# Optimization experiments

Hardware: AMD Instinct MI355X
Metric: run time of the kernel (lower is better)

The kernel has to match this reference:

```python
import jax, jax.numpy as jnp
import numpy as np

EMBED = 1024
HEADS = 16
HEAD_DIM = EMBED // HEADS


def setup_inputs() -> dict:
    key = jax.random.key(0)
    ks = jax.random.split(key, 8)
    N, L = 4, 2048
    values = jax.random.normal(ks[0], (N, L, EMBED), dtype=jnp.float32)
    keys_ = jax.random.normal(ks[1], (N, L, EMBED), dtype=jnp.float32)
    queries = jax.random.normal(ks[2], (N, L, EMBED), dtype=jnp.float32)
    s = 1.0 / np.sqrt(HEAD_DIM)
    Wv = jax.random.normal(ks[3], (HEAD_DIM, HEAD_DIM), dtype=jnp.float32) * s
    Wk = jax.random.normal(ks[4], (HEAD_DIM, HEAD_DIM), dtype=jnp.float32) * s
    Wq = jax.random.normal(ks[5], (HEAD_DIM, HEAD_DIM), dtype=jnp.float32) * s
    Wo = jax.random.normal(ks[6], (EMBED, EMBED), dtype=jnp.float32) * (1.0 / np.sqrt(EMBED))
    bo = jnp.zeros((EMBED,), dtype=jnp.float32)
    return {"values": values, "keys": keys_, "queries": queries,
            "Wv": Wv, "Wk": Wk, "Wq": Wq, "Wo": Wo, "bo": bo}


def reference(values, keys, queries, Wv, Wk, Wq, Wo, bo):
    N, L, _ = queries.shape
    # split heads: [N, L, H, D]
    v = values.reshape(N, -1, HEADS, HEAD_DIM)
    k = keys.reshape(N, -1, HEADS, HEAD_DIM)
    q = queries.reshape(N, L, HEADS, HEAD_DIM)
    # per-head linear (same [D,D] weight shared across heads), torch Linear: x @ W.T
    v = jnp.einsum('nlhd,ed->nlhe', v, Wv)
    k = jnp.einsum('nlhd,ed->nlhe', k, Wk)
    q = jnp.einsum('nqhd,ed->nqhe', q, Wq)
    # attention scores [N, H, Q, K], scaled by sqrt(embed_size) as in source
    scores = jnp.einsum('nqhd,nkhd->nhqk', q, k) / jnp.sqrt(jnp.float32(EMBED))
    attn = jax.nn.softmax(scores, axis=-1)
    out = jnp.einsum('nhqk,nkhd->nqhd', attn, v).reshape(N, L, EMBED)
    return out @ Wo.T + bo
```

## Files before the change

### kernel.cpp

```cpp
#include <hip/hip_runtime.h>
#include <math.h>

#define EMBED 1024
#define HEADS 16
#define HD    64
#define NB    4
#define LSEQ  2048

typedef __attribute__((ext_vector_type(8))) short bf16x8;
typedef __attribute__((ext_vector_type(16))) float f32x16;

typedef __attribute__((address_space(1))) void as1_void;
typedef __attribute__((address_space(3))) void as3_void;

__device__ __forceinline__ void gload_lds16(const void* g, void* l) {
    __builtin_amdgcn_global_load_lds((const as1_void*)g, (as3_void*)l, 16, 0, 0);
}

__device__ inline bf16x8 as_bf16x8(uint4 u) {
    union { uint4 u; bf16x8 b; } c; c.u = u; return c.b;
}
__device__ inline unsigned short bf16r(float x) {
    unsigned u = __float_as_uint(x);
    u += 0x7fffu + ((u >> 16) & 1u);
    return (unsigned short)(u >> 16);
}
__device__ inline float bfh2f(unsigned short h) {
    return __uint_as_float(((unsigned)h) << 16);
}
__device__ inline void split2(float x, float y, unsigned& hw, unsigned& lw) {
    unsigned short hx = bf16r(x), hy = bf16r(y);
    unsigned short lx = bf16r(x - bfh2f(hx)), ly = bf16r(y - bfh2f(hy));
    hw = (unsigned)hx | ((unsigned)hy << 16);
    lw = (unsigned)lx | ((unsigned)ly << 16);
}

__global__ __launch_bounds__(256, 3) void proj_kernel(
    const float* __restrict__ Xv, const float* __restrict__ Xk, const float* __restrict__ Xq,
    const float* __restrict__ Wv, const float* __restrict__ Wk, const float* __restrict__ Wq,
    unsigned short* __restrict__ Vt, unsigned short* __restrict__ Kp, unsigned short* __restrict__ Qp)
{
    __shared__ uint4 sXh[128 * 8];
    __shared__ uint4 sXl[128 * 8];
    __shared__ uint4 sWh[64 * 8];
    __shared__ uint4 sWl[64 * 8];

    const int t = threadIdx.x;
    const int lane = t & 63, w = t >> 6;
    const int l5 = lane & 31, hi = lane >> 5;
    const int h  = blockIdx.y;
    const int n  = blockIdx.x >> 4;
    const int l0 = (blockIdx.x & 15) * 128;

    const float QSC = 1.44269504088896341f / 32.0f;
    const float* Xs[3] = {Xv, Xk, Xq};
    const float* Ws[3] = {Wv, Wk, Wq};

    const int frow = t >> 4;
    const int fcol = t & 15;

    for (int p = 0; p < 3; ++p) {
        __syncthreads();
        {
            const float* xb = Xs[p] + ((size_t)(n * LSEQ + l0 + frow)) * EMBED + h * HD + fcol * 4;
            unsigned short* dh = (unsigned short*)sXh;
            unsigned short* dl = (unsigned short*)sXl;
            #pragma unroll
            for (int i = 0; i < 8; ++i) {
                int row = frow + i * 16;
                float4 v = *(const float4*)(xb + (size_t)i * 16 * EMBED);
                int gg = fcol >> 1, s8 = (fcol & 1) * 4;
                int idx = row * 64 + ((gg ^ (row & 7)) * 8) + s8;
                uint2 hv, lv;
                split2(v.x, v.y, hv.x, lv.x);
                split2(v.z, v.w, hv.y, lv.y);
                *(uint2*)(dh + idx) = hv;
                *(uint2*)(dl + idx) = lv;
            }
        }
        #pragma unroll
        for (int i = 0; i < 2; ++i) {
            int u = t + 256 * i;
            int e = u >> 3, g = u & 7;
            const float* wb = Ws[p] + u * 8;
            float4 v0 = *(const float4*)(wb);
            float4 v1 = *(const float4*)(wb + 4);
            uint4 hq, lq;
            split2(v0.x, v0.y, hq.x, lq.x);
            split2(v0.z, v0.w, hq.y, lq.y);
            split2(v1.x, v1.y, hq.z, lq.z);
            split2(v1.z, v1.w, hq.w, lq.w);
            int idx = e * 8 + (g ^ (e & 7));
            sWh[idx] = hq;
            sWl[idx] = lq;
        }
        __syncthreads();

        f32x16 acc0, acc1;
        #pragma unroll
        for (int i = 0; i < 16; ++i) { acc0[i] = 0.f; acc1[i] = 0.f; }

        const int xrow = w * 32 + l5;
        const int w0r = l5, w1r = 32 + l5;
        #pragma unroll
        for (int kc = 0; kc < 4; ++kc) {
            int gsel = kc * 2 + hi;
            bf16x8 xh = as_bf16x8(sXh[xrow * 8 + (gsel ^ (xrow & 7))]);
            bf16x8 xl = as_bf16x8(sXl[xrow * 8 + (gsel ^ (xrow & 7))]);
            bf16x8 wh0 = as_bf16x8(sWh[w0r * 8 + (gsel ^ (w0r & 7))]);
            bf16x8 wl0 = as_bf16x8(sWl[w0r * 8 + (gsel ^ (w0r & 7))]);
            bf16x8 wh1 = as_bf16x8(sWh[w1r * 8 + (gsel ^ (w1r & 7))]);
            bf16x8 wl1 = as_bf16x8(sWl[w1r * 8 + (gsel ^ (w1r & 7))]);
            if (p == 0) {
                acc0 = __builtin_amdgcn_mfma_f32_32x32x16_bf16(wh0, xh, acc0, 0, 0, 0);
                acc0 = __builtin_amdgcn_mfma_f32_32x32x16_bf16(wh0, xl, acc0, 0, 0, 0);
                acc0 = __builtin_amdgcn_mfma_f32_32x32x16_bf16(wl0, xh, acc0, 0, 0, 0);
                acc1 = __builtin_amdgcn_mfma_f32_32x32x16_bf16(wh1, xh, acc1, 0, 0, 0);
                acc1 = __builtin_amdgcn_mfma_f32_32x32x16_bf16(wh1, xl, acc1, 0, 0, 0);
                acc1 = __builtin_amdgcn_mfma_f32_32x32x16_bf16(wl1, xh, acc1, 0, 0, 0);
            } else {
                acc0 = __builtin_amdgcn_mfma_f32_32x32x16_bf16(xh, wh0, acc0, 0, 0, 0);
                acc0 = __builtin_amdgcn_mfma_f32_32x32x16_bf16(xh, wl0, acc0, 0, 0, 0);
                acc0 = __builtin_amdgcn_mfma_f32_32x32x16_bf16(xl, wh0, acc0, 0, 0, 0);
                acc1 = __builtin_amdgcn_mfma_f32_32x32x16_bf16(xh, wh1, acc1, 0, 0, 0);
                acc1 = __builtin_amdgcn_mfma_f32_32x32x16_bf16(xh, wl1, acc1, 0, 0, 0);
                acc1 = __builtin_amdgcn_mfma_f32_32x32x16_bf16(xl, wh1, acc1, 0, 0, 0);
            }
        }

        if (p == 0) {
            unsigned short* vb = Vt + (((size_t)(n * HEADS + h)) * HD) * LSEQ + l0 + w * 32 + l5;
            #pragma unroll
            for (int r = 0; r < 16; ++r) {
                int er = (r & 3) + 8 * (r >> 2) + 4 * hi;
                vb[(size_t)er * LSEQ]        = bf16r(acc0[r]);
                vb[(size_t)(32 + er) * LSEQ] = bf16r(acc1[r]);
            }
        } else {
            unsigned short* dst = (p == 1) ? Kp : Qp;
            float sc = (p == 2) ? QSC : 1.0f;
            unsigned short* db = dst + (((size_t)(n * HEADS + h)) * LSEQ + l0 + w * 32) * HD;
            #pragma unroll
            for (int r = 0; r < 16; ++r) {
                int tok = (r & 3) + 8 * (r >> 2) + 4 * hi;
                db[(size_t)tok * HD + l5]      = bf16r(acc0[r] * sc);
                db[(size_t)tok * HD + 32 + l5] = bf16r(acc1[r] * sc);
            }
        }
    }
}

__global__ __launch_bounds__(256, 4) void attn_kernel(
    const unsigned short* __restrict__ Qp, const unsigned short* __restrict__ Kp,
    const unsigned short* __restrict__ Vt,
    unsigned short* __restrict__ AOh, unsigned short* __restrict__ AOl)
{
    __shared__ uint4 sK[2][64 * 8];
    __shared__ uint4 sV[2][64 * 8];

    const int t = threadIdx.x;
    const int lane = t & 63, w = t >> 6;
    const int l5 = lane & 31, hi = lane >> 5;
    const int n = blockIdx.z, h = blockIdx.y;
    const int q0 = blockIdx.x * 128;
    const size_t hoff = ((size_t)n * HEADS + h) * (size_t)(LSEQ * HD);
    const unsigned short* Kh = Kp + hoff;
    const unsigned short* Vh = Vt + hoff;

    bf16x8 qf[4];
    {
        const uint4* qg = (const uint4*)(Qp + hoff + (size_t)(q0 + w * 32 + l5) * HD);
        #pragma unroll
        for (int kc = 0; kc < 4; ++kc) qf[kc] = as_bf16x8(qg[kc * 2 + hi]);
    }

    f32x16 Oa0, Oa1;
    #pragma unroll
    for (int i = 0; i < 16; ++i) { Oa0[i] = 0.f; Oa1[i] = 0.f; }
    float ls0 = 0.f, ls1 = 0.f;

    const int r0 = t >> 3;
    const int g0 = (t & 7) ^ (r0 & 7);
    const uint4* gK = (const uint4*)Kh;
    const uint4* gV = (const uint4*)Vh;

    #define STAGE(TILE, BUF)                                                        \
        do {                                                                        \
            int kb_ = (TILE) * 64;                                                  \
            gload_lds16(gK + (size_t)(kb_ + r0) * 8 + g0,        &sK[BUF][t]);      \
            gload_lds16(gK + (size_t)(kb_ + r0 + 32) * 8 + g0,   &sK[BUF][t + 256]);\
            gload_lds16(gV + (size_t)r0 * 256 + (kb_ >> 3) + g0, &sV[BUF][t]);      \
            gload_lds16(gV + (size_t)(r0 + 32) * 256 + (kb_ >> 3) + g0,             \
                        &sV[BUF][t + 256]);                                         \
        } while (0)

    STAGE(0, 0);
    int cur = 0;

    for (int tt = 0; tt < LSEQ / 64; ++tt) {
        if (tt + 1 < LSEQ / 64) {
            STAGE(tt + 1, cur ^ 1);
            asm volatile("s_waitcnt vmcnt(4)" ::: "memory");
        } else {
            asm volatile("s_waitcnt vmcnt(0)" ::: "memory");
        }
        __builtin_amdgcn_s_barrier();

        #pragma unroll
        for (int tc = 0; tc < 2; ++tc) {
            f32x16 c;
            #pragma unroll
            for (int i = 0; i < 16; ++i) c[i] = 0.f;
            int key = tc * 32 + l5;
            __builtin_amdgcn_s_setprio(1);
            #pragma unroll
            for (int kc = 0; kc < 4; ++kc) {
                bf16x8 kf = as_bf16x8(sK[cur][key * 8 + ((kc * 2 + hi) ^ (l5 & 7))]);
                c = __builtin_amdgcn_mfma_f32_32x32x16_bf16(kf, qf[kc], c, 0, 0, 0);
            }
            __builtin_amdgcn_s_setprio(0);

            unsigned pw[8];
            #pragma unroll
            for (int g = 0; g < 4; ++g) {
                float p0 = exp2f(c[4 * g]);
                float p1 = exp2f(c[4 * g + 1]);
                float p2 = exp2f(c[4 * g + 2]);
                float p3 = exp2f(c[4 * g + 3]);
                ls0 += (p0 + p1);
                ls1 += (p2 + p3);
                asm("v_cvt_pk_bf16_f32 %0, %1, %2" : "=v"(pw[2 * g])     : "v"(p0), "v"(p1));
                asm("v_cvt_pk_bf16_f32 %0, %1, %2" : "=v"(pw[2 * g + 1]) : "v"(p2), "v"(p3));
            }
            asm("v_permlane32_swap_b32 %0, %1" : "+v"(pw[0]), "+v"(pw[2]));
            asm("v_permlane32_swap_b32 %0, %1" : "+v"(pw[1]), "+v"(pw[3]));
            asm("v_permlane32_swap_b32 %0, %1" : "+v"(pw[4]), "+v"(pw[6]));
            asm("v_permlane32_swap_b32 %0, %1" : "+v"(pw[5]), "+v"(pw[7]));

            __builtin_amdgcn_s_setprio(1);
            #pragma unroll
            for (int win = 0; win < 2; ++win) {
                union { unsigned u[4]; bf16x8 b; } pf;
                pf.u[0] = pw[4 * win];
                pf.u[1] = pw[4 * win + 1];
                pf.u[2] = pw[4 * win + 2];
                pf.u[3] = pw[4 * win + 3];
                int vg = tc * 4 + (win << 1) + hi;
                bf16x8 v0 = as_bf16x8(sV[cur][ l5       * 8 + (vg ^ (l5 & 7))]);
                Oa0 = __builtin_amdgcn_mfma_f32_32x32x16_bf16(pf.b, v0, Oa0, 0, 0, 0);
                bf16x8 v1 = as_bf16x8(sV[cur][(32 + l5) * 8 + (vg ^ (l5 & 7))]);
                Oa1 = __builtin_amdgcn_mfma_f32_32x32x16_bf16(pf.b, v1, Oa1, 0, 0, 0);
            }
            __builtin_amdgcn_s_setprio(0);
        }
        __builtin_amdgcn_s_barrier();
        cur ^= 1;
    }
    #undef STAGE

    float lsum = ls0 + ls1;
    lsum += __shfl_xor(lsum, 32);
    float inv = 1.0f / lsum;
    float* sLf = (float*)&sK[0][0];
    if (hi == 0) sLf[w * 32 + l5] = inv;
    __syncthreads();

    unsigned short* hB = AOh + hoff;
    unsigned short* lB = AOl + hoff;
    #pragma unroll
    for (int r = 0; r < 16; ++r) {
        int qr = (r & 3) + 8 * (r >> 2) + 4 * hi;
        float invq = sLf[w * 32 + qr];
        size_t row = (size_t)(q0 + w * 32 + qr) * HD;
        float o0 = Oa0[r] * invq;
        float o1 = Oa1[r] * invq;
        unsigned short h0 = bf16r(o0), h1 = bf16r(o1);
        hB[row +      l5] = h0;
        hB[row + 32 + l5] = h1;
        lB[row +      l5] = bf16r(o0 - bfh2f(h0));
        lB[row + 32 + l5] = bf16r(o1 - bfh2f(h1));
    }
}

__global__ __launch_bounds__(256) void wsplit_kernel(
    const float* __restrict__ Wo,
    unsigned short* __restrict__ Woh, unsigned short* __restrict__ Wol)
{
    int i = blockIdx.x * 256 + threadIdx.x;
    float4 v = ((const float4*)Wo)[i];
    ushort4 h, l;
    h.x = bf16r(v.x); l.x = bf16r(v.x - bfh2f(h.x));
    h.y = bf16r(v.y); l.y = bf16r(v.y - bfh2f(h.y));
    h.z = bf16r(v.z); l.z = bf16r(v.z - bfh2f(h.z));
    h.w = bf16r(v.w); l.w = bf16r(v.w - bfh2f(h.w));
    ((ushort4*)Woh)[i] = h;
    ((ushort4*)Wol)[i] = l;
}

__global__ __launch_bounds__(256, 2) void outproj_kernel(
    const unsigned short* __restrict__ AOh, const unsigned short* __restrict__ AOl,
    const unsigned short* __restrict__ Woh, const unsigned short* __restrict__ Wol,
    const float* __restrict__ bo, float* __restrict__ out)
{
    __shared__ uint4 sAh[1024];
    __shared__ uint4 sAl[1024];
    __shared__ uint4 sBh[1024];
    __shared__ uint4 sBl[1024];

    const int t = threadIdx.x;
    const int lane = t & 63, w = t >> 6;
    const int l5 = lane & 31, hi = lane >> 5;
    const int m0 = blockIdx.x * 128;
    const int e0 = blockIdx.y * 128;
    const int n  = m0 >> 11, l0 = m0 & 2047;
    const int mr = (w & 1) * 64, nc = (w >> 1) * 64;

    f32x16 acc[2][2];
    #pragma unroll
    for (int a = 0; a < 2; ++a)
        #pragma unroll
        for (int b = 0; b < 2; ++b)
            #pragma unroll
            for (int i = 0; i < 16; ++i) acc[a][b][i] = 0.f;

    for (int hh = 0; hh < 16; ++hh) {
        const unsigned short* Ah = AOh + ((((size_t)n * HEADS + hh) * LSEQ) + l0) * HD;
        const unsigned short* Al = AOl + ((((size_t)n * HEADS + hh) * LSEQ) + l0) * HD;
        #pragma unroll
        for (int i = 0; i < 4; ++i) {
            int g = t + i * 256;
            gload_lds16(Ah + g * 8, sAh + g);
            gload_lds16(Al + g * 8, sAl + g);
            int e = g >> 3, gf = g & 7;
            size_t boff = (size_t)(e0 + e) * EMBED + hh * 64 + gf * 8;
            gload_lds16(Woh + boff, sBh + g);
            gload_lds16(Wol + boff, sBl + g);
        }
        __syncthreads();

        #pragma unroll
        for (int s = 0; s < 4; ++s) {
            int gcol = s * 2 + hi;
            bf16x8 ah0 = as_bf16x8(sAh[(mr +      l5) * 8 + gcol]);
            bf16x8 ah1 = as_bf16x8(sAh[(mr + 32 + l5) * 8 + gcol]);
            bf16x8 al0 = as_bf16x8(sAl[(mr +      l5) * 8 + gcol]);
            bf16x8 al1 = as_bf16x8(sAl[(mr + 32 + l5) * 8 + gcol]);
            bf16x8 bh0 = as_bf16x8(sBh[(nc +      l5) * 8 + gcol]);
            bf16x8 bh1 = as_bf16x8(sBh[(nc + 32 + l5) * 8 + gcol]);
            bf16x8 bl0 = as_bf16x8(sBl[(nc +      l5) * 8 + gcol]);
            bf16x8 bl1 = as_bf16x8(sBl[(nc + 32 + l5) * 8 + gcol]);

            acc[0][0] = __builtin_amdgcn_mfma_f32_32x32x16_bf16(ah0, bh0, acc[0][0], 0, 0, 0);
            acc[0][1] = __builtin_amdgcn_mfma_f32_32x32x16_bf16(ah0, bh1, acc[0][1], 0, 0, 0);
            acc[1][0] = __builtin_amdgcn_mfma_f32_32x32x16_bf16(ah1, bh0, acc[1][0], 0, 0, 0);
            acc[1][1] = __builtin_amdgcn_mfma_f32_32x32x16_bf16(ah1, bh1, acc[1][1], 0, 0, 0);

            acc[0][0] = __builtin_amdgcn_mfma_f32_32x32x16_bf16(ah0, bl0, acc[0][0], 0, 0, 0);
            acc[0][1] = __builtin_amdgcn_mfma_f32_32x32x16_bf16(ah0, bl1, acc[0][1], 0, 0, 0);
            acc[1][0] = __builtin_amdgcn_mfma_f32_32x32x16_bf16(ah1, bl0, acc[1][0], 0, 0, 0);
            acc[1][1] = __builtin_amdgcn_mfma_f32_32x32x16_bf16(ah1, bl1, acc[1][1], 0, 0, 0);

            acc[0][0] = __builtin_amdgcn_mfma_f32_32x32x16_bf16(al0, bh0, acc[0][0], 0, 0, 0);
            acc[0][1] = __builtin_amdgcn_mfma_f32_32x32x16_bf16(al0, bh1, acc[0][1], 0, 0, 0);
            acc[1][0] = __builtin_amdgcn_mfma_f32_32x32x16_bf16(al1, bh0, acc[1][0], 0, 0, 0);
            acc[1][1] = __builtin_amdgcn_mfma_f32_32x32x16_bf16(al1, bh1, acc[1][1], 0, 0, 0);
        }
        __syncthreads();
    }

    float b0 = bo[e0 + nc + l5];
    float b1 = bo[e0 + nc + 32 + l5];
    #pragma unroll
    for (int ti = 0; ti < 2; ++ti) {
        #pragma unroll
        for (int r = 0; r < 16; ++r) {
            int row = m0 + mr + ti * 32 + (r & 3) + 8 * (r >> 2) + 4 * hi;
            float* o = out + (size_t)row * EMBED + e0 + nc;
            o[l5]      = acc[ti][0][r] + b0;
            o[32 + l5] = acc[ti][1][r] + b1;
        }
    }
}

extern "C" void kernel_launch(void* const* d_in, const int* in_sizes, int n_in,
                              void* d_out, int out_size, void* d_ws, size_t ws_size,
                              hipStream_t stream)
{
    const float* values  = (const float*)d_in[0];
    const float* keys    = (const float*)d_in[1];
    const float* queries = (const float*)d_in[2];
    const float* Wv      = (const float*)d_in[3];
    const float* Wk      = (const float*)d_in[4];
    const float* Wq      = (const float*)d_in[5];
    const float* Wo      = (const float*)d_in[6];
    const float* bo      = (const float*)d_in[7];
    float* out = (float*)d_out;

    const size_t bufElems = (size_t)NB * HEADS * LSEQ * HD;
    unsigned short* Qp  = (unsigned short*)d_ws;
    unsigned short* Kp  = Qp  + bufElems;
    unsigned short* Vt  = Kp  + bufElems;
    unsigned short* AOh = Vt  + bufElems;
    unsigned short* AOl = AOh + bufElems;
    unsigned short* Woh = AOl + bufElems;
    unsigned short* Wol = Woh + (size_t)EMBED * EMBED;

    wsplit_kernel<<<dim3(1024), 256, 0, stream>>>(Wo, Woh, Wol);
    proj_kernel<<<dim3(NB * 16, HEADS), 256, 0, stream>>>(values, keys, queries, Wv, Wk, Wq, Vt, Kp, Qp);
    attn_kernel<<<dim3(LSEQ / 128, HEADS, NB), 256, 0, stream>>>(Qp, Kp, Vt, AOh, AOl);
    outproj_kernel<<<dim3(NB * LSEQ / 128, EMBED / 128), 256, 0, stream>>>(AOh, AOl, Woh, Wol, bo, out);
}
```

Measured before the change: 377.9 us.

## Double-buffer out-projection LDS stages and prefetch next QKV projection inputs

The output-projection GEMM now splits each head's K=64 slice into two 32-wide chunks and double-buffers them in LDS. The next chunk's global-to-LDS loads are issued before computing the current one, with vmcnt-based waits and an XOR swizzle to reduce bank conflicts. The QKV projection kernel prefetches the next projection's X and W tiles into registers while the current one computes. This trades extra registers and a subtler barrier/waitcnt protocol for hiding global load latency.

```diff
diff --git a/kernel.cpp b/kernel.cpp
--- a/kernel.cpp
+++ b/kernel.cpp
@@ -59,21 +59,34 @@
     const int frow = t >> 4;
     const int fcol = t & 15;
 
+    float4 xr[8];
+    float4 wr[4];
+
+    {
+        const float* xb = Xs[0] + ((size_t)(n * LSEQ + l0 + frow)) * EMBED + h * HD + fcol * 4;
+        #pragma unroll
+        for (int i = 0; i < 8; ++i) xr[i] = *(const float4*)(xb + (size_t)i * 16 * EMBED);
+        const float* wb0 = Ws[0] + (size_t)t * 8;
+        const float* wb1 = Ws[0] + (size_t)(t + 256) * 8;
+        wr[0] = *(const float4*)(wb0);
+        wr[1] = *(const float4*)(wb0 + 4);
+        wr[2] = *(const float4*)(wb1);
+        wr[3] = *(const float4*)(wb1 + 4);
+    }
+
     for (int p = 0; p < 3; ++p) {
         __syncthreads();
         {
-            const float* xb = Xs[p] + ((size_t)(n * LSEQ + l0 + frow)) * EMBED + h * HD + fcol * 4;
             unsigned short* dh = (unsigned short*)sXh;
             unsigned short* dl = (unsigned short*)sXl;
             #pragma unroll
             for (int i = 0; i < 8; ++i) {
                 int row = frow + i * 16;
-                float4 v = *(const float4*)(xb + (size_t)i * 16 * EMBED);
                 int gg = fcol >> 1, s8 = (fcol & 1) * 4;
                 int idx = row * 64 + ((gg ^ (row & 7)) * 8) + s8;
                 uint2 hv, lv;
-                split2(v.x, v.y, hv.x, lv.x);
-                split2(v.z, v.w, hv.y, lv.y);
+                split2(xr[i].x, xr[i].y, hv.x, lv.x);
+                split2(xr[i].z, xr[i].w, hv.y, lv.y);
                 *(uint2*)(dh + idx) = hv;
                 *(uint2*)(dl + idx) = lv;
             }
@@ -82,19 +95,28 @@
         for (int i = 0; i < 2; ++i) {
             int u = t + 256 * i;
             int e = u >> 3, g = u & 7;
-            const float* wb = Ws[p] + u * 8;
-            float4 v0 = *(const float4*)(wb);
-            float4 v1 = *(const float4*)(wb + 4);
             uint4 hq, lq;
-            split2(v0.x, v0.y, hq.x, lq.x);
-            split2(v0.z, v0.w, hq.y, lq.y);
-            split2(v1.x, v1.y, hq.z, lq.z);
-            split2(v1.z, v1.w, hq.w, lq.w);
+            split2(wr[2 * i].x, wr[2 * i].y, hq.x, lq.x);
+            split2(wr[2 * i].z, wr[2 * i].w, hq.y, lq.y);
+            split2(wr[2 * i + 1].x, wr[2 * i + 1].y, hq.z, lq.z);
+            split2(wr[2 * i + 1].z, wr[2 * i + 1].w, hq.w, lq.w);
             int idx = e * 8 + (g ^ (e & 7));
             sWh[idx] = hq;
             sWl[idx] = lq;
         }
-        __syncthreads();
+        if (p < 2) {
+            const float* xb = Xs[p + 1] + ((size_t)(n * LSEQ + l0 + frow)) * EMBED + h * HD + fcol * 4;
+            #pragma unroll
+            for (int i = 0; i < 8; ++i) xr[i] = *(const float4*)(xb + (size_t)i * 16 * EMBED);
+            const float* wb0 = Ws[p + 1] + (size_t)t * 8;
+            const float* wb1 = Ws[p + 1] + (size_t)(t + 256) * 8;
+            wr[0] = *(const float4*)(wb0);
+            wr[1] = *(const float4*)(wb0 + 4);
+            wr[2] = *(const float4*)(wb1);
+            wr[3] = *(const float4*)(wb1 + 4);
+        }
+        asm volatile("s_waitcnt lgkmcnt(0)" ::: "memory");
+        __builtin_amdgcn_s_barrier();
 
         f32x16 acc0, acc1;
         #pragma unroll
@@ -302,10 +324,10 @@
     const unsigned short* __restrict__ Woh, const unsigned short* __restrict__ Wol,
     const float* __restrict__ bo, float* __restrict__ out)
 {
-    __shared__ uint4 sAh[1024];
-    __shared__ uint4 sAl[1024];
-    __shared__ uint4 sBh[1024];
-    __shared__ uint4 sBl[1024];
+    __shared__ uint4 sAh[2][512];
+    __shared__ uint4 sAl[2][512];
+    __shared__ uint4 sBh[2][512];
+    __shared__ uint4 sBl[2][512];
 
     const int t = threadIdx.x;
     const int lane = t & 63, w = t >> 6;
@@ -315,6 +337,28 @@
     const int n  = m0 >> 11, l0 = m0 & 2047;
     const int mr = (w & 1) * 64, nc = (w >> 1) * 64;
 
+    const int ar0 = t >> 2;
+    const int ag0 = (t & 3) ^ (ar0 & 3);
+
+    #define OSTAGE(C, BUF)                                                            \
+        do {                                                                          \
+            int hh_ = (C) >> 1, hf_ = (C) & 1;                                        \
+            const uint4* gAh_ = (const uint4*)(AOh) +                                 \
+                (((size_t)n * HEADS + hh_) * LSEQ + l0) * 8;                          \
+            const uint4* gAl_ = (const uint4*)(AOl) +                                 \
+                (((size_t)n * HEADS + hh_) * LSEQ + l0) * 8;                          \
+            const uint4* gBh_ = (const uint4*)(Woh) + (size_t)e0 * 128 + hh_ * 8;     \
+            const uint4* gBl_ = (const uint4*)(Wol) + (size_t)e0 * 128 + hh_ * 8;     \
+            gload_lds16(gAh_ + (size_t)ar0 * 8 + hf_ * 4 + ag0,        &sAh[BUF][t]);       \
+            gload_lds16(gAh_ + (size_t)(ar0 + 64) * 8 + hf_ * 4 + ag0, &sAh[BUF][t + 256]); \
+            gload_lds16(gAl_ + (size_t)ar0 * 8 + hf_ * 4 + ag0,        &sAl[BUF][t]);       \
+            gload_lds16(gAl_ + (size_t)(ar0 + 64) * 8 + hf_ * 4 + ag0, &sAl[BUF][t + 256]); \
+            gload_lds16(gBh_ + (size_t)ar0 * 128 + hf_ * 4 + ag0,        &sBh[BUF][t]);       \
+            gload_lds16(gBh_ + (size_t)(ar0 + 64) * 128 + hf_ * 4 + ag0, &sBh[BUF][t + 256]); \
+            gload_lds16(gBl_ + (size_t)ar0 * 128 + hf_ * 4 + ag0,        &sBl[BUF][t]);       \
+            gload_lds16(gBl_ + (size_t)(ar0 + 64) * 128 + hf_ * 4 + ag0, &sBl[BUF][t + 256]); \
+        } while (0)
+
     f32x16 acc[2][2];
     #pragma unroll
     for (int a = 0; a < 2; ++a)
@@ -323,32 +367,30 @@
             #pragma unroll
             for (int i = 0; i < 16; ++i) acc[a][b][i] = 0.f;
 
-    for (int hh = 0; hh < 16; ++hh) {
-        const unsigned short* Ah = AOh + ((((size_t)n * HEADS + hh) * LSEQ) + l0) * HD;
-        const unsigned short* Al = AOl + ((((size_t)n * HEADS + hh) * LSEQ) + l0) * HD;
-        #pragma unroll
-        for (int i = 0; i < 4; ++i) {
-            int g = t + i * 256;
-            gload_lds16(Ah + g * 8, sAh + g);
-            gload_lds16(Al + g * 8, sAl + g);
-            int e = g >> 3, gf = g & 7;
-            size_t boff = (size_t)(e0 + e) * EMBED + hh * 64 + gf * 8;
-            gload_lds16(Woh + boff, sBh + g);
-            gload_lds16(Wol + boff, sBl + g);
-        }
-        __syncthreads();
-
-        #pragma unroll
-        for (int s = 0; s < 4; ++s) {
-            int gcol = s * 2 + hi;
-            bf16x8 ah0 = as_bf16x8(sAh[(mr +      l5) * 8 + gcol]);
-            bf16x8 ah1 = as_bf16x8(sAh[(mr + 32 + l5) * 8 + gcol]);
-            bf16x8 al0 = as_bf16x8(sAl[(mr +      l5) * 8 + gcol]);
-            bf16x8 al1 = as_bf16x8(sAl[(mr + 32 + l5) * 8 + gcol]);
-            bf16x8 bh0 = as_bf16x8(sBh[(nc +      l5) * 8 + gcol]);
-            bf16x8 bh1 = as_bf16x8(sBh[(nc + 32 + l5) * 8 + gcol]);
-            bf16x8 bl0 = as_bf16x8(sBl[(nc +      l5) * 8 + gcol]);
-            bf16x8 bl1 = as_bf16x8(sBl[(nc + 32 + l5) * 8 + gcol]);
+    OSTAGE(0, 0);
+    int cur = 0;
+
+    for (int c = 0; c < 32; ++c) {
+        if (c + 1 < 32) {
+            OSTAGE(c + 1, cur ^ 1);
+            asm volatile("s_waitcnt vmcnt(8)" ::: "memory");
+        } else {
+            asm volatile("s_waitcnt vmcnt(0)" ::: "memory");
+        }
+        __builtin_amdgcn_s_barrier();
+
+        __builtin_amdgcn_s_setprio(1);
+        #pragma unroll
+        for (int s = 0; s < 2; ++s) {
+            int gx = (s * 2 + hi) ^ (l5 & 3);
+            bf16x8 ah0 = as_bf16x8(sAh[cur][(mr +      l5) * 4 + gx]);
+            bf16x8 ah1 = as_bf16x8(sAh[cur][(mr + 32 + l5) * 4 + gx]);
+            bf16x8 al0 = as_bf16x8(sAl[cur][(mr +      l5) * 4 + gx]);
+            bf16x8 al1 = as_bf16x8(sAl[cur][(mr + 32 + l5) * 4 + gx]);
+            bf16x8 bh0 = as_bf16x8(sBh[cur][(nc +      l5) * 4 + gx]);
+            bf16x8 bh1 = as_bf16x8(sBh[cur][(nc + 32 + l5) * 4 + gx]);
+            bf16x8 bl0 = as_bf16x8(sBl[cur][(nc +      l5) * 4 + gx]);
+            bf16x8 bl1 = as_bf16x8(sBl[cur][(nc + 32 + l5) * 4 + gx]);
 
             acc[0][0] = __builtin_amdgcn_mfma_f32_32x32x16_bf16(ah0, bh0, acc[0][0], 0, 0, 0);
             acc[0][1] = __builtin_amdgcn_mfma_f32_32x32x16_bf16(ah0, bh1, acc[0][1], 0, 0, 0);
@@ -365,8 +407,11 @@
             acc[1][0] = __builtin_amdgcn_mfma_f32_32x32x16_bf16(al1, bh0, acc[1][0], 0, 0, 0);
             acc[1][1] = __builtin_amdgcn_mfma_f32_32x32x16_bf16(al1, bh1, acc[1][1], 0, 0, 0);
         }
-        __syncthreads();
-    }
+        __builtin_amdgcn_s_setprio(0);
+        __builtin_amdgcn_s_barrier();
+        cur ^= 1;
+    }
+    #undef OSTAGE
 
     float b0 = bo[e0 + nc + l5];
     float b1 = bo[e0 + nc + 32 + l5];
```

Result: faster. 363.0 us (-4.0%).

## Parallelize projection over Q/K/V and double-buffer out-projection with smaller tiles

Applied to the files above, without the earlier changes.

The projection kernel now gives each of Q, K and V its own grid slice along z, replacing the sequential loop over three inputs and tripling block count. The output projection shrinks its tile to 128x64 with a 32-deep K step. It double-buffers LDS loads with async global_load_lds, explicit vmcnt waits and raised priority around the MFMAs. The aim is more parallelism and overlap of memory with compute, at the cost of more per-block overhead and more barriers.

```diff
diff --git a/kernel.cpp b/kernel.cpp
--- a/kernel.cpp
+++ b/kernel.cpp
@@ -51,101 +51,99 @@
     const int h  = blockIdx.y;
     const int n  = blockIdx.x >> 4;
     const int l0 = (blockIdx.x & 15) * 128;
+    const int p  = blockIdx.z;
 
     const float QSC = 1.44269504088896341f / 32.0f;
-    const float* Xs[3] = {Xv, Xk, Xq};
-    const float* Ws[3] = {Wv, Wk, Wq};
+    const float* Xp = (p == 0) ? Xv : (p == 1) ? Xk : Xq;
+    const float* Wp = (p == 0) ? Wv : (p == 1) ? Wk : Wq;
 
     const int frow = t >> 4;
     const int fcol = t & 15;
 
-    for (int p = 0; p < 3; ++p) {
-        __syncthreads();
-        {
-            const float* xb = Xs[p] + ((size_t)(n * LSEQ + l0 + frow)) * EMBED + h * HD + fcol * 4;
-            unsigned short* dh = (unsigned short*)sXh;
-            unsigned short* dl = (unsigned short*)sXl;
-            #pragma unroll
-            for (int i = 0; i < 8; ++i) {
-                int row = frow + i * 16;
-                float4 v = *(const float4*)(xb + (size_t)i * 16 * EMBED);
-                int gg = fcol >> 1, s8 = (fcol & 1) * 4;
-                int idx = row * 64 + ((gg ^ (row & 7)) * 8) + s8;
-                uint2 hv, lv;
-                split2(v.x, v.y, hv.x, lv.x);
-                split2(v.z, v.w, hv.y, lv.y);
-                *(uint2*)(dh + idx) = hv;
-                *(uint2*)(dl + idx) = lv;
-            }
-        }
-        #pragma unroll
-        for (int i = 0; i < 2; ++i) {
-            int u = t + 256 * i;
-            int e = u >> 3, g = u & 7;
-            const float* wb = Ws[p] + u * 8;
-            float4 v0 = *(const float4*)(wb);
-            float4 v1 = *(const float4*)(wb + 4);
-            uint4 hq, lq;
-            split2(v0.x, v0.y, hq.x, lq.x);
-            split2(v0.z, v0.w, hq.y, lq.y);
-            split2(v1.x, v1.y, hq.z, lq.z);
-            split2(v1.z, v1.w, hq.w, lq.w);
-            int idx = e * 8 + (g ^ (e & 7));
-            sWh[idx] = hq;
-            sWl[idx] = lq;
-        }
-        __syncthreads();
-
-        f32x16 acc0, acc1;
-        #pragma unroll
-        for (int i = 0; i < 16; ++i) { acc0[i] = 0.f; acc1[i] = 0.f; }
-
-        const int xrow = w * 32 + l5;
-        const int w0r = l5, w1r = 32 + l5;
-        #pragma unroll
-        for (int kc = 0; kc < 4; ++kc) {
-            int gsel = kc * 2 + hi;
-            bf16x8 xh = as_bf16x8(sXh[xrow * 8 + (gsel ^ (xrow & 7))]);
-            bf16x8 xl = as_bf16x8(sXl[xrow * 8 + (gsel ^ (xrow & 7))]);
-            bf16x8 wh0 = as_bf16x8(sWh[w0r * 8 + (gsel ^ (w0r & 7))]);
-            bf16x8 wl0 = as_bf16x8(sWl[w0r * 8 + (gsel ^ (w0r & 7))]);
-            bf16x8 wh1 = as_bf16x8(sWh[w1r * 8 + (gsel ^ (w1r & 7))]);
-            bf16x8 wl1 = as_bf16x8(sWl[w1r * 8 + (gsel ^ (w1r & 7))]);
-            if (p == 0) {
-                acc0 = __builtin_amdgcn_mfma_f32_32x32x16_bf16(wh0, xh, acc0, 0, 0, 0);
-                acc0 = __builtin_amdgcn_mfma_f32_32x32x16_bf16(wh0, xl, acc0, 0, 0, 0);
-                acc0 = __builtin_amdgcn_mfma_f32_32x32x16_bf16(wl0, xh, acc0, 0, 0, 0);
-                acc1 = __builtin_amdgcn_mfma_f32_32x32x16_bf16(wh1, xh, acc1, 0, 0, 0);
-                acc1 = __builtin_amdgcn_mfma_f32_32x32x16_bf16(wh1, xl, acc1, 0, 0, 0);
-                acc1 = __builtin_amdgcn_mfma_f32_32x32x16_bf16(wl1, xh, acc1, 0, 0, 0);
-            } else {
-                acc0 = __builtin_amdgcn_mfma_f32_32x32x16_bf16(xh, wh0, acc0, 0, 0, 0);
-                acc0 = __builtin_amdgcn_mfma_f32_32x32x16_bf16(xh, wl0, acc0, 0, 0, 0);
-                acc0 = __builtin_amdgcn_mfma_f32_32x32x16_bf16(xl, wh0, acc0, 0, 0, 0);
-                acc1 = __builtin_amdgcn_mfma_f32_32x32x16_bf16(xh, wh1, acc1, 0, 0, 0);
-                acc1 = __builtin_amdgcn_mfma_f32_32x32x16_bf16(xh, wl1, acc1, 0, 0, 0);
-                acc1 = __builtin_amdgcn_mfma_f32_32x32x16_bf16(xl, wh1, acc1, 0, 0, 0);
-            }
-        }
-
+    {
+        const float* xb = Xp + ((size_t)(n * LSEQ + l0 + frow)) * EMBED + h * HD + fcol * 4;
+        unsigned short* dh = (unsigned short*)sXh;
+        unsigned short* dl = (unsigned short*)sXl;
+        #pragma unroll
+        for (int i = 0; i < 8; ++i) {
+            int row = frow + i * 16;
+            float4 v = *(const float4*)(xb + (size_t)i * 16 * EMBED);
+            int gg = fcol >> 1, s8 = (fcol & 1) * 4;
+            int idx = row * 64 + ((gg ^ (row & 7)) * 8) + s8;
+            uint2 hv, lv;
+            split2(v.x, v.y, hv.x, lv.x);
+            split2(v.z, v.w, hv.y, lv.y);
+            *(uint2*)(dh + idx) = hv;
+            *(uint2*)(dl + idx) = lv;
+        }
+    }
+    #pragma unroll
+    for (int i = 0; i < 2; ++i) {
+        int u = t + 256 * i;
+        int e = u >> 3, g = u & 7;
+        const float* wb = Wp + u * 8;
+        float4 v0 = *(const float4*)(wb);
+        float4 v1 = *(const float4*)(wb + 4);
+        uint4 hq, lq;
+        split2(v0.x, v0.y, hq.x, lq.x);
+        split2(v0.z, v0.w, hq.y, lq.y);
+        split2(v1.x, v1.y, hq.z, lq.z);
+        split2(v1.z, v1.w, hq.w, lq.w);
+        int idx = e * 8 + (g ^ (e & 7));
+        sWh[idx] = hq;
+        sWl[idx] = lq;
+    }
+    __syncthreads();
+
+    f32x16 acc0, acc1;
+    #pragma unroll
+    for (int i = 0; i < 16; ++i) { acc0[i] = 0.f; acc1[i] = 0.f; }
+
+    const int xrow = w * 32 + l5;
+    const int w0r = l5, w1r = 32 + l5;
+    #pragma unroll
+    for (int kc = 0; kc < 4; ++kc) {
+        int gsel = kc * 2 + hi;
+        bf16x8 xh = as_bf16x8(sXh[xrow * 8 + (gsel ^ (xrow & 7))]);
+        bf16x8 xl = as_bf16x8(sXl[xrow * 8 + (gsel ^ (xrow & 7))]);
+        bf16x8 wh0 = as_bf16x8(sWh[w0r * 8 + (gsel ^ (w0r & 7))]);
+        bf16x8 wl0 = as_bf16x8(sWl[w0r * 8 + (gsel ^ (w0r & 7))]);
+        bf16x8 wh1 = as_bf16x8(sWh[w1r * 8 + (gsel ^ (w1r & 7))]);
+        bf16x8 wl1 = as_bf16x8(sWl[w1r * 8 + (gsel ^ (w1r & 7))]);
         if (p == 0) {
-            unsigned short* vb = Vt + (((size_t)(n * HEADS + h)) * HD) * LSEQ + l0 + w * 32 + l5;
-            #pragma unroll
-            for (int r = 0; r < 16; ++r) {
-                int er = (r & 3) + 8 * (r >> 2) + 4 * hi;
-                vb[(size_t)er * LSEQ]        = bf16r(acc0[r]);
-                vb[(size_t)(32 + er) * LSEQ] = bf16r(acc1[r]);
-            }
+            acc0 = __builtin_amdgcn_mfma_f32_32x32x16_bf16(wh0, xh, acc0, 0, 0, 0);
+            acc0 = __builtin_amdgcn_mfma_f32_32x32x16_bf16(wh0, xl, acc0, 0, 0, 0);
+            acc0 = __builtin_amdgcn_mfma_f32_32x32x16_bf16(wl0, xh, acc0, 0, 0, 0);
+            acc1 = __builtin_amdgcn_mfma_f32_32x32x16_bf16(wh1, xh, acc1, 0, 0, 0);
+            acc1 = __builtin_amdgcn_mfma_f32_32x32x16_bf16(wh1, xl, acc1, 0, 0, 0);
+            acc1 = __builtin_amdgcn_mfma_f32_32x32x16_bf16(wl1, xh, acc1, 0, 0, 0);
         } else {
-            unsigned short* dst = (p == 1) ? Kp : Qp;
-            float sc = (p == 2) ? QSC : 1.0f;
-            unsigned short* db = dst + (((size_t)(n * HEADS + h)) * LSEQ + l0 + w * 32) * HD;
-            #pragma unroll
-            for (int r = 0; r < 16; ++r) {
-                int tok = (r & 3) + 8 * (r >> 2) + 4 * hi;
-                db[(size_t)tok * HD + l5]      = bf16r(acc0[r] * sc);
-                db[(size_t)tok * HD + 32 + l5] = bf16r(acc1[r] * sc);
-            }
+            acc0 = __builtin_amdgcn_mfma_f32_32x32x16_bf16(xh, wh0, acc0, 0, 0, 0);
+            acc0 = __builtin_amdgcn_mfma_f32_32x32x16_bf16(xh, wl0, acc0, 0, 0, 0);
+            acc0 = __builtin_amdgcn_mfma_f32_32x32x16_bf16(xl, wh0, acc0, 0, 0, 0);
+            acc1 = __builtin_amdgcn_mfma_f32_32x32x16_bf16(xh, wh1, acc1, 0, 0, 0);
+            acc1 = __builtin_amdgcn_mfma_f32_32x32x16_bf16(xh, wl1, acc1, 0, 0, 0);
+            acc1 = __builtin_amdgcn_mfma_f32_32x32x16_bf16(xl, wh1, acc1, 0, 0, 0);
+        }
+    }
+
+    if (p == 0) {
+        unsigned short* vb = Vt + (((size_t)(n * HEADS + h)) * HD) * LSEQ + l0 + w * 32 + l5;
+        #pragma unroll
+        for (int r = 0; r < 16; ++r) {
+            int er = (r & 3) + 8 * (r >> 2) + 4 * hi;
+            vb[(size_t)er * LSEQ]        = bf16r(acc0[r]);
+            vb[(size_t)(32 + er) * LSEQ] = bf16r(acc1[r]);
+        }
+    } else {
+        unsigned short* dst = (p == 1) ? Kp : Qp;
+        float sc = (p == 2) ? QSC : 1.0f;
+        unsigned short* db = dst + (((size_t)(n * HEADS + h)) * LSEQ + l0 + w * 32) * HD;
+        #pragma unroll
+        for (int r = 0; r < 16; ++r) {
+            int tok = (r & 3) + 8 * (r >> 2) + 4 * hi;
+            db[(size_t)tok * HD + l5]      = bf16r(acc0[r] * sc);
+            db[(size_t)tok * HD + 32 + l5] = bf16r(acc1[r] * sc);
         }
     }
 }
@@ -297,88 +295,94 @@
     ((ushort4*)Wol)[i] = l;
 }
 
-__global__ __launch_bounds__(256, 2) void outproj_kernel(
+__global__ __launch_bounds__(256, 3) void outproj_kernel(
     const unsigned short* __restrict__ AOh, const unsigned short* __restrict__ AOl,
     const unsigned short* __restrict__ Woh, const unsigned short* __restrict__ Wol,
     const float* __restrict__ bo, float* __restrict__ out)
 {
-    __shared__ uint4 sAh[1024];
-    __shared__ uint4 sAl[1024];
-    __shared__ uint4 sBh[1024];
-    __shared__ uint4 sBl[1024];
+    __shared__ uint4 sAh[2][512];
+    __shared__ uint4 sAl[2][512];
+    __shared__ uint4 sBh[2][256];
+    __shared__ uint4 sBl[2][256];
 
     const int t = threadIdx.x;
     const int lane = t & 63, w = t >> 6;
     const int l5 = lane & 31, hi = lane >> 5;
     const int m0 = blockIdx.x * 128;
-    const int e0 = blockIdx.y * 128;
+    const int e0 = blockIdx.y * 64;
     const int n  = m0 >> 11, l0 = m0 & 2047;
-    const int mr = (w & 1) * 64, nc = (w >> 1) * 64;
-
-    f32x16 acc[2][2];
-    #pragma unroll
-    for (int a = 0; a < 2; ++a)
-        #pragma unroll
-        for (int b = 0; b < 2; ++b)
-            #pragma unroll
-            for (int i = 0; i < 16; ++i) acc[a][b][i] = 0.f;
-
-    for (int hh = 0; hh < 16; ++hh) {
-        const unsigned short* Ah = AOh + ((((size_t)n * HEADS + hh) * LSEQ) + l0) * HD;
-        const unsigned short* Al = AOl + ((((size_t)n * HEADS + hh) * LSEQ) + l0) * HD;
-        #pragma unroll
-        for (int i = 0; i < 4; ++i) {
-            int g = t + i * 256;
-            gload_lds16(Ah + g * 8, sAh + g);
-            gload_lds16(Al + g * 8, sAl + g);
-            int e = g >> 3, gf = g & 7;
-            size_t boff = (size_t)(e0 + e) * EMBED + hh * 64 + gf * 8;
-            gload_lds16(Woh + boff, sBh + g);
-            gload_lds16(Wol + boff, sBl + g);
-        }
-        __syncthreads();
-
-        #pragma unroll
-        for (int s = 0; s < 4; ++s) {
-            int gcol = s * 2 + hi;
-            bf16x8 ah0 = as_bf16x8(sAh[(mr +      l5) * 8 + gcol]);
-            bf16x8 ah1 = as_bf16x8(sAh[(mr + 32 + l5) * 8 + gcol]);
-            bf16x8 al0 = as_bf16x8(sAl[(mr +      l5) * 8 + gcol]);
-            bf16x8 al1 = as_bf16x8(sAl[(mr + 32 + l5) * 8 + gcol]);
-            bf16x8 bh0 = as_bf16x8(sBh[(nc +      l5) * 8 + gcol]);
-            bf16x8 bh1 = as_bf16x8(sBh[(nc + 32 + l5) * 8 + gcol]);
-            bf16x8 bl0 = as_bf16x8(sBl[(nc +      l5) * 8 + gcol]);
-            bf16x8 bl1 = as_bf16x8(sBl[(nc + 32 + l5) * 8 + gcol]);
-
-            acc[0][0] = __builtin_amdgcn_mfma_f32_32x32x16_bf16(ah0, bh0, acc[0][0], 0, 0, 0);
-            acc[0][1] = __builtin_amdgcn_mfma_f32_32x32x16_bf16(ah0, bh1, acc[0][1], 0, 0, 0);
-            acc[1][0] = __builtin_amdgcn_mfma_f32_32x32x16_bf16(ah1, bh0, acc[1][0], 0, 0, 0);
-            acc[1][1] = __builtin_amdgcn_mfma_f32_32x32x16_bf16(ah1, bh1, acc[1][1], 0, 0, 0);
-
-            acc[0][0] = __builtin_amdgcn_mfma_f32_32x32x16_bf16(ah0, bl0, acc[0][0], 0, 0, 0);
-            acc[0][1] = __builtin_amdgcn_mfma_f32_32x32x16_bf16(ah0, bl1, acc[0][1], 0, 0, 0);
-            acc[1][0] = __builtin_amdgcn_mfma_f32_32x32x16_bf16(ah1, bl0, acc[1][0], 0, 0, 0);
-            acc[1][1] = __builtin_amdgcn_mfma_f32_32x32x16_bf16(ah1, bl1, acc[1][1], 0, 0, 0);
-
-            acc[0][0] = __builtin_amdgcn_mfma_f32_32x32x16_bf16(al0, bh0, acc[0][0], 0, 0, 0);
-            acc[0][1] = __builtin_amdgcn_mfma_f32_32x32x16_bf16(al0, bh1, acc[0][1], 0, 0, 0);
-            acc[1][0] = __builtin_amdgcn_mfma_f32_32x32x16_bf16(al1, bh0, acc[1][0], 0, 0, 0);
-            acc[1][1] = __builtin_amdgcn_mfma_f32_32x32x16_bf16(al1, bh1, acc[1][1], 0, 0, 0);
-        }
-        __syncthreads();
-    }
-
-    float b0 = bo[e0 + nc + l5];
-    float b1 = bo[e0 + nc + 32 + l5];
-    #pragma unroll
-    for (int ti = 0; ti < 2; ++ti) {
-        #pragma unroll
-        for (int r = 0; r < 16; ++r) {
-            int row = m0 + mr + ti * 32 + (r & 3) + 8 * (r >> 2) + 4 * hi;
-            float* o = out + (size_t)row * EMBED + e0 + nc;
-            o[l5]      = acc[ti][0][r] + b0;
-            o[32 + l5] = acc[ti][1][r] + b1;
-        }
+
+    const int arow = t >> 2;
+    const int aswz = (t & 3) ^ (arow & 3);
+
+    #define OSTAGE(C, BUF)                                                            \
+        do {                                                                          \
+            int hh_ = (C) >> 1, hf_ = (C) & 1;                                        \
+            const uint4* gAh_ = (const uint4*)(AOh) +                                 \
+                (((size_t)n * HEADS + hh_) * LSEQ + l0) * 8 + hf_ * 4;                \
+            const uint4* gAl_ = (const uint4*)(AOl) +                                 \
+                (((size_t)n * HEADS + hh_) * LSEQ + l0) * 8 + hf_ * 4;                \
+            const uint4* gBh_ = (const uint4*)(Woh) +                                 \
+                (size_t)(e0 + arow) * 128 + hh_ * 8 + hf_ * 4;                        \
+            const uint4* gBl_ = (const uint4*)(Wol) +                                 \
+                (size_t)(e0 + arow) * 128 + hh_ * 8 + hf_ * 4;                        \
+            gload_lds16(gAh_ + (size_t)arow * 8 + aswz,        &sAh[BUF][t]);         \
+            gload_lds16(gAh_ + (size_t)(arow + 64) * 8 + aswz, &sAh[BUF][t + 256]);   \
+            gload_lds16(gAl_ + (size_t)arow * 8 + aswz,        &sAl[BUF][t]);         \
+            gload_lds16(gAl_ + (size_t)(arow + 64) * 8 + aswz, &sAl[BUF][t + 256]);   \
+            gload_lds16(gBh_ + aswz, &sBh[BUF][t]);                                   \
+            gload_lds16(gBl_ + aswz, &sBl[BUF][t]);                                   \
+        } while (0)
+
+    f32x16 acc0, acc1;
+    #pragma unroll
+    for (int i = 0; i < 16; ++i) { acc0[i] = 0.f; acc1[i] = 0.f; }
+
+    OSTAGE(0, 0);
+    int cur = 0;
+
+    const int amr = w * 32 + l5;
+    for (int c = 0; c < 32; ++c) {
+        if (c + 1 < 32) {
+            OSTAGE(c + 1, cur ^ 1);
+            asm volatile("s_waitcnt vmcnt(6)" ::: "memory");
+        } else {
+            asm volatile("s_waitcnt vmcnt(0)" ::: "memory");
+        }
+        __builtin_amdgcn_s_barrier();
+
+        __builtin_amdgcn_s_setprio(1);
+        #pragma unroll
+        for (int ks = 0; ks < 2; ++ks) {
+            int gx = ks * 2 + hi;
+            bf16x8 ah = as_bf16x8(sAh[cur][amr * 4 + (gx ^ (amr & 3))]);
+            bf16x8 al = as_bf16x8(sAl[cur][amr * 4 + (gx ^ (amr & 3))]);
+            bf16x8 bh0 = as_bf16x8(sBh[cur][ l5       * 4 + (gx ^ (l5 & 3))]);
+            bf16x8 bh1 = as_bf16x8(sBh[cur][(32 + l5) * 4 + (gx ^ (l5 & 3))]);
+            bf16x8 bl0 = as_bf16x8(sBl[cur][ l5       * 4 + (gx ^ (l5 & 3))]);
+            bf16x8 bl1 = as_bf16x8(sBl[cur][(32 + l5) * 4 + (gx ^ (l5 & 3))]);
+
+            acc0 = __builtin_amdgcn_mfma_f32_32x32x16_bf16(ah, bh0, acc0, 0, 0, 0);
+            acc1 = __builtin_amdgcn_mfma_f32_32x32x16_bf16(ah, bh1, acc1, 0, 0, 0);
+            acc0 = __builtin_amdgcn_mfma_f32_32x32x16_bf16(ah, bl0, acc0, 0, 0, 0);
+            acc1 = __builtin_amdgcn_mfma_f32_32x32x16_bf16(ah, bl1, acc1, 0, 0, 0);
+            acc0 = __builtin_amdgcn_mfma_f32_32x32x16_bf16(al, bh0, acc0, 0, 0, 0);
+            acc1 = __builtin_amdgcn_mfma_f32_32x32x16_bf16(al, bh1, acc1, 0, 0, 0);
+        }
+        __builtin_amdgcn_s_setprio(0);
+        __builtin_amdgcn_s_barrier();
+        cur ^= 1;
+    }
+    #undef OSTAGE
+
+    float b0 = bo[e0 + l5];
+    float b1 = bo[e0 + 32 + l5];
+    #pragma unroll
+    for (int r = 0; r < 16; ++r) {
+        int row = m0 + w * 32 + (r & 3) + 8 * (r >> 2) + 4 * hi;
+        float* o = out + (size_t)row * EMBED + e0;
+        o[l5]      = acc0[r] + b0;
+        o[32 + l5] = acc1[r] + b1;
     }
 }
 
@@ -406,7 +410,7 @@
     unsigned short* Wol = Woh + (size_t)EMBED * EMBED;
 
     wsplit_kernel<<<dim3(1024), 256, 0, stream>>>(Wo, Woh, Wol);
-    proj_kernel<<<dim3(NB * 16, HEADS), 256, 0, stream>>>(values, keys, queries, Wv, Wk, Wq, Vt, Kp, Qp);
+    proj_kernel<<<dim3(NB * 16, HEADS, 3), 256, 0, stream>>>(values, keys, queries, Wv, Wk, Wq, Vt, Kp, Qp);
     attn_kernel<<<dim3(LSEQ / 128, HEADS, NB), 256, 0, stream>>>(Qp, Kp, Vt, AOh, AOl);
-    outproj_kernel<<<dim3(NB * LSEQ / 128, EMBED / 128), 256, 0, stream>>>(AOh, AOl, Woh, Wol, bo, out);
-}
+    outproj_kernel<<<dim3(NB * LSEQ / 128, EMBED / 64), 256, 0, stream>>>(AOh, AOl, Woh, Wol, bo, out);
+}
```

Result: faster. 352.5 us (-6.7%).
